# Performance work log

Hardware: AMD Instinct MI355X
Metric: run time of the kernel (lower is better)

The kernel has to match this reference:

```python
import jax, jax.numpy as jnp
import numpy as np

TOP_K = 2


def layer_norm(x, g, b, eps=1e-5):
    m = jnp.mean(x, axis=-1, keepdims=True)
    v = jnp.mean((x - m) ** 2, axis=-1, keepdims=True)
    return (x - m) * jax.lax.rsqrt(v + eps) * g + b


def setup_inputs() -> dict:
    key = jax.random.key(0)
    ks = jax.random.split(key, 6)
    B, P, D, E, K = 8, 1024, 1024, 8, TOP_K
    x = jax.random.normal(ks[0], (B, P, D), dtype=jnp.float32)
    noise = jax.random.normal(ks[1], (B * P * K, D), dtype=jnp.float32) * 1e-5
    Wg = jax.random.normal(ks[2], (D, E), dtype=jnp.float32) * 0.02
    bg = jnp.zeros((E,), dtype=jnp.float32)
    W1 = jax.random.normal(ks[3], (E, D, D), dtype=jnp.float32) * 0.02
    b1 = jnp.zeros((E, D), dtype=jnp.float32)
    W2 = jax.random.normal(ks[4], (E, D, D), dtype=jnp.float32) * 0.02
    b2 = jnp.zeros((E, D), dtype=jnp.float32)
    ln_g = jnp.ones((E, D), dtype=jnp.float32)
    ln_b = jnp.zeros((E, D), dtype=jnp.float32)
    gn_g = jnp.ones((D,), dtype=jnp.float32)
    gn_b = jnp.zeros((D,), dtype=jnp.float32)
    return {"x": x, "noise": noise, "Wg": Wg, "bg": bg, "W1": W1, "b1": b1,
            "W2": W2, "b2": b2, "ln_g": ln_g, "ln_b": ln_b, "gn_g": gn_g, "gn_b": gn_b}


def reference(x, noise, Wg, bg, W1, b1, W2, b2, ln_g, ln_b, gn_g, gn_b):
    # Eval-mode forward of Allocator (aux_loss == 0, not returned).
    B, P, D = x.shape
    E = Wg.shape[1]
    K = TOP_K
    N = B * P
    logits = jnp.einsum('bpd,de->bpe', x, Wg) + bg          # [B,P,E]
    probs = jax.nn.softmax(logits, axis=-1).reshape(N, E)
    _topk_probs, topk_idx = jax.lax.top_k(probs, K)          # probs unused in eval combine
    flat_idx = topk_idx.reshape(-1)                          # [N*K]
    sample_idx = jnp.repeat(jnp.arange(N), K)                # [N*K]
    batch_idx = sample_idx // P                              # [N*K]
    xg = x.reshape(N, D)[sample_idx] + noise                 # [N*K, D] gathered token copies
    sums = []
    for e in range(E):  # fixed small expert loop
        h = jax.nn.gelu(xg @ W1[e] + b1[e], approximate=False)
        y = h @ W2[e] + b2[e] + xg                           # Mlp + residual
        y = layer_norm(y, ln_g[e], ln_b[e])                  # Expert.norm
        m = (flat_idx == e)[:, None]
        # one_hot(batch_idx).T @ masked_output == per-batch segment sum (unweighted)
        sums.append(jax.ops.segment_sum(jnp.where(m, y, 0.0), batch_idx, num_segments=B))
    out = jnp.stack(sums, axis=0).transpose(1, 0, 2)         # [B, E, D]
    return layer_norm(out, gn_g, gn_b)
```

## Files before the change

### kernel.cpp

```cpp
#include <hip/hip_runtime.h>
#include <hip/hip_bf16.h>
#include <math.h>

#define D 1024
#define NTOK 8192
#define NSLOT 16384
#define NGRP 64
#define MAXTILE 136

typedef short bf16x8 __attribute__((ext_vector_type(8)));
typedef float floatx4 __attribute__((ext_vector_type(4)));

__device__ __forceinline__ unsigned short f2bf(float f) {
    __hip_bfloat16 h = __float2bfloat16(f);
    return *reinterpret_cast<unsigned short*>(&h);
}
__device__ __forceinline__ float bf2f(unsigned short u) {
    unsigned int v = ((unsigned int)u) << 16;
    return __uint_as_float(v);
}

__device__ __forceinline__ void load_lds16(const void* g, void* l) {
    __builtin_amdgcn_global_load_lds(
        (const __attribute__((address_space(1))) unsigned int*)g,
        (__attribute__((address_space(3))) unsigned int*)l, 16, 0, 0);
}

__global__ void zero_kernel(int* __restrict__ grp_cnt, float* __restrict__ S) {
    int i = blockIdx.x * 256 + threadIdx.x;
    if (i < NGRP) grp_cnt[i] = 0;
    if (i < 64 * D) S[i] = 0.f;
}

__global__ void route_kernel(const float* __restrict__ x, const float* __restrict__ Wg,
                             const float* __restrict__ bg, int* __restrict__ slot_e,
                             int* __restrict__ grp_cnt) {
    int wave = threadIdx.x >> 6;
    int lane = threadIdx.x & 63;
    int tok = blockIdx.x * 4 + wave;
    const float* xr = x + (size_t)tok * D;
    float acc[8] = {0.f,0.f,0.f,0.f,0.f,0.f,0.f,0.f};
    for (int k = lane; k < D; k += 64) {
        float xv = xr[k];
        const float4* w4 = reinterpret_cast<const float4*>(Wg + k * 8);
        float4 a = w4[0], b = w4[1];
        acc[0] += xv * a.x; acc[1] += xv * a.y; acc[2] += xv * a.z; acc[3] += xv * a.w;
        acc[4] += xv * b.x; acc[5] += xv * b.y; acc[6] += xv * b.z; acc[7] += xv * b.w;
    }
#pragma unroll
    for (int e = 0; e < 8; e++) {
#pragma unroll
        for (int off = 32; off > 0; off >>= 1)
            acc[e] += __shfl_xor(acc[e], off, 64);
    }
    if (lane == 0) {
        float lg[8];
#pragma unroll
        for (int e = 0; e < 8; e++) lg[e] = acc[e] + bg[e];
        int e1 = 0; float b1v = lg[0];
#pragma unroll
        for (int e = 1; e < 8; e++) if (lg[e] > b1v) { b1v = lg[e]; e1 = e; }
        int e2 = -1; float b2v = -3.0e38f;
#pragma unroll
        for (int e = 0; e < 8; e++) { if (e == e1) continue; if (lg[e] > b2v) { b2v = lg[e]; e2 = e; } }
        int b = tok >> 10;
        slot_e[2 * tok] = e1;
        slot_e[2 * tok + 1] = e2;
        atomicAdd(&grp_cnt[e1 * 8 + b], 1);
        atomicAdd(&grp_cnt[e2 * 8 + b], 1);
    }
}

__global__ void prefix_kernel(const int* __restrict__ grp_cnt, int* __restrict__ goff,
                              int* __restrict__ cursor, int2* __restrict__ tile_tab) {
    if (threadIdx.x != 0) return;
    int s = 0;
    for (int g = 0; g < NGRP; g++) { goff[g] = s; cursor[g] = s; s += grp_cnt[g]; }
    goff[NGRP] = s;
    int t = 0;
    for (int e = 0; e < 8; e++) {
        int cnt = goff[e * 8 + 8] - goff[e * 8];
        for (int m0 = 0; m0 < cnt; m0 += 128) tile_tab[t++] = make_int2(e, m0);
    }
    for (; t < MAXTILE; t++) tile_tab[t] = make_int2(-1, 0);
}

__global__ void build_xg_kernel(const float* __restrict__ x, const float* __restrict__ noise,
                                const int* __restrict__ slot_e, int* __restrict__ cursor,
                                unsigned short* __restrict__ xg) {
    int wave = threadIdx.x >> 6;
    int lane = threadIdx.x & 63;
    int slot = blockIdx.x * 4 + wave;
    int e = slot_e[slot];
    int b = slot >> 11;
    int row = 0;
    if (lane == 0) row = atomicAdd(&cursor[e * 8 + b], 1);
    row = __shfl(row, 0, 64);
    int tok = slot >> 1;
    const float4* xr = reinterpret_cast<const float4*>(x + (size_t)tok * D);
    const float4* nr = reinterpret_cast<const float4*>(noise + (size_t)slot * D);
    ushort4* og = reinterpret_cast<ushort4*>(xg + (size_t)row * D);
    for (int i = lane; i < D / 4; i += 64) {
        float4 a = xr[i], n = nr[i];
        ushort4 o;
        o.x = f2bf(a.x + n.x); o.y = f2bf(a.y + n.y);
        o.z = f2bf(a.z + n.z); o.w = f2bf(a.w + n.w);
        og[i] = o;
    }
}

__global__ void wconv_kernel(const float* __restrict__ W1, const float* __restrict__ W2,
                             unsigned short* __restrict__ W1t, unsigned short* __restrict__ W2t) {
    int z = blockIdx.y;
    int mat = z & 1, e = z >> 1;
    const float* src = (mat ? W2 : W1) + (size_t)e * D * D;
    unsigned short* dst = (mat ? W2t : W1t) + (size_t)e * D * D;
    int kc = blockIdx.x;
    int tid = threadIdx.x;
#pragma unroll
    for (int p = 0; p < 4; p++) {
        int n = p * 256 + tid;
#pragma unroll
        for (int kb = 0; kb < 8; kb++) {
            int kbase = kc * 64 + kb * 8;
            unsigned int w[4];
#pragma unroll
            for (int kk = 0; kk < 4; kk++) {
                unsigned short lo = f2bf(src[(size_t)(kbase + 2 * kk) * D + n]);
                unsigned short hi = f2bf(src[(size_t)(kbase + 2 * kk + 1) * D + n]);
                w[kk] = (unsigned int)lo | ((unsigned int)hi << 16);
            }
            uint4 o = make_uint4(w[0], w[1], w[2], w[3]);
            *reinterpret_cast<uint4*>(dst + (size_t)(kbase >> 3) * (D * 8) + (size_t)n * 8) = o;
        }
    }
}

template <int MODE>
__global__ __launch_bounds__(256)
void gemm_kernel(const unsigned short* __restrict__ A,
                 const unsigned short* __restrict__ Wt,
                 const float* __restrict__ bias,
                 const unsigned short* __restrict__ xg,
                 const int2* __restrict__ tile_tab,
                 const int* __restrict__ goff,
                 unsigned short* __restrict__ Hout) {
    __shared__ unsigned short As[2][128 * 32];
    __shared__ unsigned short Bs[2][64 * 32];

    int2 tt = tile_tab[blockIdx.y];
    int e = tt.x;
    if (e < 0) return;
    int m0 = tt.y;
    int rowBase = goff[e * 8];
    int cnt = goff[e * 8 + 8] - rowBase;
    int n0 = blockIdx.x * 64;

    int tid = threadIdx.x;
    int lane = tid & 63, wave = tid >> 6;
    int wm = wave >> 1, wn = wave & 1;
    int lr = lane & 15, quad = lane >> 4;
    int l2 = lane >> 2, l4 = lane & 3;

    int arow0 = min(m0 + (wave * 2 + 0) * 16 + l2, cnt - 1);
    int arow1 = min(m0 + (wave * 2 + 1) * 16 + l2, cnt - 1);
    const unsigned short* ap0 = A + ((size_t)(rowBase + arow0) << 10) + l4 * 8;
    const unsigned short* ap1 = A + ((size_t)(rowBase + arow1) << 10) + l4 * 8;
    const unsigned short* bp = Wt + (size_t)e * D * D
                               + (size_t)l4 * (D * 8)
                               + (size_t)(n0 + wave * 16 + l2) * 8;

    unsigned short* a_dst0[2] = { &As[0][(wave * 2 + 0) * 512 + lane * 8],
                                  &As[1][(wave * 2 + 0) * 512 + lane * 8] };
    unsigned short* a_dst1[2] = { &As[0][(wave * 2 + 1) * 512 + lane * 8],
                                  &As[1][(wave * 2 + 1) * 512 + lane * 8] };
    unsigned short* b_dst[2]  = { &Bs[0][wave * 512 + lane * 8],
                                  &Bs[1][wave * 512 + lane * 8] };

    const unsigned short* a_frag = &As[0][(wm * 64 + lr) * 32 + quad * 8];
    const unsigned short* b_frag = &Bs[0][(wn * 32 + lr) * 32 + quad * 8];

    floatx4 acc[4][2] = {};

    load_lds16(ap0, a_dst0[0]); load_lds16(ap1, a_dst1[0]); load_lds16(bp, b_dst[0]);
    ap0 += 32; ap1 += 32; bp += 4 * D * 8;

#pragma unroll 1
    for (int k0 = 0; k0 < D; k0 += 64) {
        __syncthreads();
        if (k0 + 32 < D) {
            load_lds16(ap0, a_dst0[1]); load_lds16(ap1, a_dst1[1]); load_lds16(bp, b_dst[1]);
            ap0 += 32; ap1 += 32; bp += 4 * D * 8;
        }
        {
            bf16x8 af[4], bfr[2];
#pragma unroll
            for (int i = 0; i < 4; i++)
                af[i] = *reinterpret_cast<const bf16x8*>(a_frag + i * 512);
#pragma unroll
            for (int j = 0; j < 2; j++)
                bfr[j] = *reinterpret_cast<const bf16x8*>(b_frag + j * 512);
#pragma unroll
            for (int i = 0; i < 4; i++)
#pragma unroll
                for (int j = 0; j < 2; j++)
                    acc[i][j] = __builtin_amdgcn_mfma_f32_16x16x32_bf16(af[i], bfr[j], acc[i][j], 0, 0, 0);
        }
        __syncthreads();
        if (k0 + 64 < D) {
            load_lds16(ap0, a_dst0[0]); load_lds16(ap1, a_dst1[0]); load_lds16(bp, b_dst[0]);
            ap0 += 32; ap1 += 32; bp += 4 * D * 8;
        }
        {
            bf16x8 af[4], bfr[2];
#pragma unroll
            for (int i = 0; i < 4; i++)
                af[i] = *reinterpret_cast<const bf16x8*>(a_frag + 4096 + i * 512);
#pragma unroll
            for (int j = 0; j < 2; j++)
                bfr[j] = *reinterpret_cast<const bf16x8*>(b_frag + 2048 + j * 512);
#pragma unroll
            for (int i = 0; i < 4; i++)
#pragma unroll
                for (int j = 0; j < 2; j++)
                    acc[i][j] = __builtin_amdgcn_mfma_f32_16x16x32_bf16(af[i], bfr[j], acc[i][j], 0, 0, 0);
        }
    }

#pragma unroll
    for (int i = 0; i < 4; i++) {
        int rowb = m0 + wm * 64 + i * 16 + quad * 4;
#pragma unroll
        for (int j = 0; j < 2; j++) {
            int col = n0 + wn * 32 + j * 16 + lr;
            float bia = bias[e * D + col];
#pragma unroll
            for (int r = 0; r < 4; r++) {
                int rr = rowb + r;
                if (rr < cnt) {
                    float v = acc[i][j][r] + bia;
                    size_t idx = (size_t)(rowBase + rr) * D + col;
                    if (MODE == 0) {
                        float g = 0.5f * v * (1.0f + erff(v * 0.70710678118654752f));
                        Hout[idx] = f2bf(g);
                    } else {
                        v += bf2f(xg[idx]);
                        Hout[idx] = f2bf(v);
                    }
                }
            }
        }
    }
}

__global__ void lnsum_kernel(const unsigned short* __restrict__ ybf,
                             const int* __restrict__ goff, float* __restrict__ S) {
    int grp = blockIdx.x, chunk = blockIdx.y;
    int r0 = goff[grp] + chunk * 64;
    int r1 = min(goff[grp + 1], r0 + 64);
    if (r0 >= r1) return;
    __shared__ float part[D];
    for (int i = threadIdx.x; i < D; i += 256) part[i] = 0.f;
    __syncthreads();

    int wave = threadIdx.x >> 6, lane = threadIdx.x & 63;
    float p[16] = {0.f};
    for (int r = r0 + wave; r < r1; r += 4) {
        const unsigned short* row = ybf + ((size_t)r << 10);
        float v[16];
        float s = 0.f, sq = 0.f;
#pragma unroll
        for (int c = 0; c < 4; c++) {
            ushort4 u = *reinterpret_cast<const ushort4*>(row + c * 256 + lane * 4);
            float a = bf2f(u.x), b = bf2f(u.y), cc = bf2f(u.z), d = bf2f(u.w);
            v[c * 4 + 0] = a; v[c * 4 + 1] = b; v[c * 4 + 2] = cc; v[c * 4 + 3] = d;
            s += a + b + cc + d;
            sq += a * a + b * b + cc * cc + d * d;
        }
#pragma unroll
        for (int off = 32; off > 0; off >>= 1) {
            s += __shfl_xor(s, off, 64);
            sq += __shfl_xor(sq, off, 64);
        }
        float m = s * (1.f / 1024.f);
        float rs = rsqrtf(sq * (1.f / 1024.f) - m * m + 1e-5f);
#pragma unroll
        for (int c = 0; c < 16; c++) p[c] += (v[c] - m) * rs;
    }
#pragma unroll
    for (int c = 0; c < 4; c++)
#pragma unroll
        for (int q = 0; q < 4; q++)
            atomicAdd(&part[c * 256 + lane * 4 + q], p[c * 4 + q]);
    __syncthreads();

    int e = grp >> 3, b = grp & 7;
    float* Sp = S + (size_t)(b * 8 + e) * D;
    for (int i = threadIdx.x; i < D; i += 256)
        atomicAdd(&Sp[i], part[i]);
}

__global__ void finalize_kernel(const float* __restrict__ S, const int* __restrict__ goff,
                                const float* __restrict__ ln_g, const float* __restrict__ ln_b,
                                const float* __restrict__ gn_g, const float* __restrict__ gn_b,
                                float* __restrict__ out) {
    int be = blockIdx.x;
    int b = be >> 3, e = be & 7;
    int grp = e * 8 + b;
    float cnt = (float)(goff[grp + 1] - goff[grp]);
    int tid = threadIdx.x;
    __shared__ float red[8];
    float val[4];
    float s = 0.f, sq = 0.f;
#pragma unroll
    for (int c = 0; c < 4; c++) {
        int d = tid * 4 + c;
        float v = S[(size_t)be * D + d] * ln_g[e * D + d] + cnt * ln_b[e * D + d];
        val[c] = v; s += v; sq += v * v;
    }
#pragma unroll
    for (int off = 32; off > 0; off >>= 1) {
        s += __shfl_xor(s, off, 64);
        sq += __shfl_xor(sq, off, 64);
    }
    int wave = tid >> 6, lane = tid & 63;
    if (lane == 0) { red[wave] = s; red[4 + wave] = sq; }
    __syncthreads();
    float ts = red[0] + red[1] + red[2] + red[3];
    float tq = red[4] + red[5] + red[6] + red[7];
    float m = ts / 1024.f;
    float var = tq / 1024.f - m * m;
    float rstd = rsqrtf(var + 1e-5f);
#pragma unroll
    for (int c = 0; c < 4; c++) {
        int d = tid * 4 + c;
        out[(size_t)be * D + d] = (val[c] - m) * rstd * gn_g[d] + gn_b[d];
    }
}

extern "C" void kernel_launch(void* const* d_in, const int* in_sizes, int n_in,
                              void* d_out, int out_size, void* d_ws, size_t ws_size,
                              hipStream_t stream) {
    const float* x     = (const float*)d_in[0];
    const float* noise = (const float*)d_in[1];
    const float* Wg    = (const float*)d_in[2];
    const float* bg    = (const float*)d_in[3];
    const float* W1    = (const float*)d_in[4];
    const float* b1    = (const float*)d_in[5];
    const float* W2    = (const float*)d_in[6];
    const float* b2    = (const float*)d_in[7];
    const float* ln_g  = (const float*)d_in[8];
    const float* ln_b  = (const float*)d_in[9];
    const float* gn_g  = (const float*)d_in[10];
    const float* gn_b  = (const float*)d_in[11];
    float* out = (float*)d_out;

    char* ws = (char*)d_ws;
    size_t off = 0;
    unsigned short* xg   = (unsigned short*)(ws + off); off += (size_t)NSLOT * D * 2;
    unsigned short* hb   = (unsigned short*)(ws + off); off += (size_t)NSLOT * D * 2;
    unsigned short* ybf  = (unsigned short*)(ws + off); off += (size_t)NSLOT * D * 2;
    unsigned short* W1t  = (unsigned short*)(ws + off); off += (size_t)8 * D * D * 2;
    unsigned short* W2t  = (unsigned short*)(ws + off); off += (size_t)8 * D * D * 2;
    int* slot_e          = (int*)(ws + off);            off += (size_t)NSLOT * 4;
    int* grp_cnt         = (int*)(ws + off);            off += 256;
    int* goff            = (int*)(ws + off);            off += 512;
    int* cursor          = (int*)(ws + off);            off += 256;
    int2* tile_tab       = (int2*)(ws + off);           off += MAXTILE * 8;
    float* S             = (float*)(ws + off);          off += (size_t)64 * D * 4;

    zero_kernel<<<256, 256, 0, stream>>>(grp_cnt, S);
    route_kernel<<<NTOK / 4, 256, 0, stream>>>(x, Wg, bg, slot_e, grp_cnt);
    prefix_kernel<<<1, 64, 0, stream>>>(grp_cnt, goff, cursor, tile_tab);
    wconv_kernel<<<dim3(16, 16), 256, 0, stream>>>(W1, W2, W1t, W2t);
    build_xg_kernel<<<NSLOT / 4, 256, 0, stream>>>(x, noise, slot_e, cursor, xg);
    gemm_kernel<0><<<dim3(16, MAXTILE), 256, 0, stream>>>(xg, W1t, b1, xg, tile_tab, goff, hb);
    gemm_kernel<1><<<dim3(16, MAXTILE), 256, 0, stream>>>(hb, W2t, b2, xg, tile_tab, goff, ybf);
    lnsum_kernel<<<dim3(64, 16), 256, 0, stream>>>(ybf, goff, S);
    finalize_kernel<<<64, 256, 0, stream>>>(S, goff, ln_g, ln_b, gn_g, gn_b, out);
}
```

Measured before the change: 587.2 us.

## Remap GEMM blocks for XCD locality and parallelize weight conversion

The GEMM grid becomes 1D and block ids are remapped so each XCD handles whole row tiles across all 16 column tiles. Blocks sharing an A tile then land on the same XCD and can reuse it in that XCD's L2. The weight-conversion kernel is rewritten to use 8x more blocks, with each thread doing vectorized float4 row loads and a register transpose instead of strided scalar loads. The lnsum grid is also doubled in y. The mapping assumes round-robin dispatch of blocks across 8 XCDs and that MAXTILE is a multiple of 8.

New measurement: 538.6 us. 1.09x faster.

```diff
diff --git a/kernel.cpp b/kernel.cpp
--- a/kernel.cpp
+++ b/kernel.cpp
@@ -113,26 +113,25 @@
                              unsigned short* __restrict__ W1t, unsigned short* __restrict__ W2t) {
     int z = blockIdx.y;
     int mat = z & 1, e = z >> 1;
-    const float* src = (mat ? W2 : W1) + (size_t)e * D * D;
-    unsigned short* dst = (mat ? W2t : W1t) + (size_t)e * D * D;
-    int kc = blockIdx.x;
-    int tid = threadIdx.x;
-#pragma unroll
-    for (int p = 0; p < 4; p++) {
-        int n = p * 256 + tid;
-#pragma unroll
-        for (int kb = 0; kb < 8; kb++) {
-            int kbase = kc * 64 + kb * 8;
-            unsigned int w[4];
-#pragma unroll
-            for (int kk = 0; kk < 4; kk++) {
-                unsigned short lo = f2bf(src[(size_t)(kbase + 2 * kk) * D + n]);
-                unsigned short hi = f2bf(src[(size_t)(kbase + 2 * kk + 1) * D + n]);
-                w[kk] = (unsigned int)lo | ((unsigned int)hi << 16);
-            }
-            uint4 o = make_uint4(w[0], w[1], w[2], w[3]);
-            *reinterpret_cast<uint4*>(dst + (size_t)(kbase >> 3) * (D * 8) + (size_t)n * 8) = o;
-        }
+    int kb = blockIdx.x;
+    const float* src = (mat ? W2 : W1) + (size_t)e * D * D + (size_t)kb * 8 * D;
+    unsigned short* dst = (mat ? W2t : W1t) + (size_t)e * D * D + (size_t)kb * (D * 8);
+    int t = threadIdx.x;
+    float4 v[8];
+#pragma unroll
+    for (int k = 0; k < 8; k++)
+        v[k] = reinterpret_cast<const float4*>(src + (size_t)k * D)[t];
+    const float* vf = reinterpret_cast<const float*>(v);
+#pragma unroll
+    for (int c = 0; c < 4; c++) {
+        unsigned int w[4];
+#pragma unroll
+        for (int j = 0; j < 4; j++) {
+            unsigned short lo = f2bf(vf[(2 * j) * 4 + c]);
+            unsigned short hi = f2bf(vf[(2 * j + 1) * 4 + c]);
+            w[j] = (unsigned int)lo | ((unsigned int)hi << 16);
+        }
+        *reinterpret_cast<uint4*>(dst + (size_t)(t * 4 + c) * 8) = make_uint4(w[0], w[1], w[2], w[3]);
     }
 }
 
@@ -148,13 +147,18 @@
     __shared__ unsigned short As[2][128 * 32];
     __shared__ unsigned short Bs[2][64 * 32];
 
-    int2 tt = tile_tab[blockIdx.y];
+    int id = blockIdx.x;
+    int xcd = id & 7;
+    int rem = id >> 3;
+    int ntile = rem & 15;
+    int t = xcd + 8 * (rem >> 4);
+    int2 tt = tile_tab[t];
     int e = tt.x;
     if (e < 0) return;
     int m0 = tt.y;
     int rowBase = goff[e * 8];
     int cnt = goff[e * 8 + 8] - rowBase;
-    int n0 = blockIdx.x * 64;
+    int n0 = ntile * 64;
 
     int tid = threadIdx.x;
     int lane = tid & 63, wave = tid >> 6;
@@ -372,10 +376,10 @@
     zero_kernel<<<256, 256, 0, stream>>>(grp_cnt, S);
     route_kernel<<<NTOK / 4, 256, 0, stream>>>(x, Wg, bg, slot_e, grp_cnt);
     prefix_kernel<<<1, 64, 0, stream>>>(grp_cnt, goff, cursor, tile_tab);
-    wconv_kernel<<<dim3(16, 16), 256, 0, stream>>>(W1, W2, W1t, W2t);
+    wconv_kernel<<<dim3(128, 16), 256, 0, stream>>>(W1, W2, W1t, W2t);
     build_xg_kernel<<<NSLOT / 4, 256, 0, stream>>>(x, noise, slot_e, cursor, xg);
-    gemm_kernel<0><<<dim3(16, MAXTILE), 256, 0, stream>>>(xg, W1t, b1, xg, tile_tab, goff, hb);
-    gemm_kernel<1><<<dim3(16, MAXTILE), 256, 0, stream>>>(hb, W2t, b2, xg, tile_tab, goff, ybf);
-    lnsum_kernel<<<dim3(64, 16), 256, 0, stream>>>(ybf, goff, S);
+    gemm_kernel<0><<<dim3(2176), 256, 0, stream>>>(xg, W1t, b1, xg, tile_tab, goff, hb);
+    gemm_kernel<1><<<dim3(2176), 256, 0, stream>>>(hb, W2t, b2, xg, tile_tab, goff, ybf);
+    lnsum_kernel<<<dim3(64, 32), 256, 0, stream>>>(ybf, goff, S);
     finalize_kernel<<<64, 256, 0, stream>>>(S, goff, ln_g, ln_b, gn_g, gn_b, out);
 }
```
